# Kernel optimization log

Measured on AMD Instinct MI355X. Metric: run time of the kernel, lower is better.

The kernel has to match this reference:

```python
import jax, jax.numpy as jnp
import numpy as np

N_NODE = 40000  # item vocabulary
H = 100         # hidden size (SR-GNN default)
B = 64          # sessions per batch
L = 16          # items per session (equal-length sessions)
N = B * L       # total graph nodes
E = 2048        # total edges
NL = 1          # GatedGraphConv layers


def setup_inputs() -> dict:
    key = jax.random.key(0)
    ks = jax.random.split(key, 20)
    stdv = 1.0 / np.sqrt(H)
    u = lambda k, shape: jax.random.uniform(k, shape, jnp.float32, -stdv, stdv)
    return {
        "x": jax.random.randint(ks[0], (N,), 0, N_NODE),
        "edge_index": jax.random.randint(ks[1], (2, E), 0, N),
        "edge_weight": jax.random.uniform(ks[2], (E,), jnp.float32),
        "batch": jnp.arange(N) // L,  # node -> session id, equal-length sessions
        "embed": u(ks[3], (N_NODE, H)),
        "ggc_w": u(ks[4], (NL, H, H)),
        "gru_wih": u(ks[5], (3 * H, H)),
        "gru_whh": u(ks[6], (3 * H, H)),
        "gru_bih": u(ks[7], (3 * H,)),
        "gru_bhh": u(ks[8], (3 * H,)),
        "W1_w": u(ks[9], (H, H)), "W1_b": u(ks[10], (H,)),
        "W2_w": u(ks[11], (H, H)), "W2_b": u(ks[12], (H,)),
        "Wt_w": u(ks[13], (H, H)), "Wt_b": u(ks[14], (H,)),
        "q_w": u(ks[15], (1, H)), "q_b": u(ks[16], (1,)),
        "W3_w": u(ks[17], (H, 2 * H)), "W3_b": u(ks[18], (H,)),
    }


def reference(x, edge_index, edge_weight, batch, embed, ggc_w, gru_wih, gru_whh,
              gru_bih, gru_bhh, W1_w, W1_b, W2_w, W2_b, Wt_w, Wt_b, q_w, q_b,
              W3_w, W3_b):
    # Embedding lookup
    h = embed[x]  # [N, H]
    src, dst = edge_index[0], edge_index[1]
    # GatedGraphConv: weighted message aggregation + GRUCell update
    for l in range(NL):
        m = h @ ggc_w[l]                                             # [N, H]
        agg = jnp.zeros_like(h).at[dst].add(edge_weight[:, None] * m[src])
        gi = agg @ gru_wih.T + gru_bih                               # [N, 3H]
        gh = h @ gru_whh.T + gru_bhh
        ir, iz, inn = jnp.split(gi, 3, axis=-1)
        hr, hz, hn = jnp.split(gh, 3, axis=-1)
        r = jax.nn.sigmoid(ir + hr)
        zg = jax.nn.sigmoid(iz + hz)
        ng = jnp.tanh(inn + r * hn)
        h = (1.0 - zg) * ng + zg * h
    v = h.reshape(B, L, H)                                           # sessions
    s_l = v[:, -1]                                                   # [B, H] last item
    # alpha = q(sigmoid(W1(v_n) + W2(v)))
    a = jax.nn.sigmoid((s_l @ W1_w.T + W1_b)[:, None, :] + (v @ W2_w.T + W2_b))
    alpha = a @ q_w.T + q_b                                          # [B, L, 1]
    s_g = jnp.sum(alpha * v, axis=1)                                 # [B, H]
    s_h = jnp.concatenate([s_l, s_g], axis=-1) @ W3_w.T + W3_b       # [B, H]
    # Target attention: s_t[b] = softmax(E @ W_t(v_b)^T, -1) @ v_b, contracted
    # directly against E to avoid materializing [B, N_NODE, H].
    vt = v @ Wt_w.T + Wt_b                                           # [B, L, H]
    P = jax.nn.softmax(jnp.einsum('jh,blh->bjl', embed, vt), axis=-1)
    C = jnp.einsum('blh,jh->bjl', v, embed)                          # v_l . E_j
    z = s_h @ embed.T + jnp.sum(P * C, axis=-1)                      # [B, N_NODE]
    return z
```

## Files before the change

### kernel.cpp

```cpp
#include <hip/hip_runtime.h>
#include <hip/hip_bf16.h>

#define Hh    100
#define NN    1024
#define BB    64
#define LL    16
#define EE    2048
#define NNODE 40000

#define BSPL  4
#define BPB   (BB / BSPL)
#define PFR   8
#define PPAN  (PFR * 64 * 8)
#define GJ    4
#define EBS   104
#define GRB   4

typedef unsigned short u16;
typedef __attribute__((ext_vector_type(8))) short short8;
typedef __attribute__((ext_vector_type(4))) float f32x4;

__device__ __forceinline__ float bf2f(u16 u) {
    union { unsigned int i; float f; } v;
    v.i = ((unsigned int)u) << 16;
    return v.f;
}

__device__ __forceinline__ u16 f2bf(float f) {
    unsigned int x = __float_as_uint(f);
    unsigned int lsb = (x >> 16) & 1u;
    x += 0x7fffu + lsb;
    return (u16)(x >> 16);
}

__device__ __forceinline__ float sigmoidf_(float x) {
    return 1.0f / (1.0f + expf(-x));
}

template <bool BF>
__device__ __forceinline__ float ldv(const void* p, size_t i) {
    if (BF) return bf2f(((const u16*)p)[i]);
    return ((const float*)p)[i];
}
__device__ __forceinline__ float ldvf(int flag, const void* p, size_t i) {
    return flag ? ldv<true>(p, i) : ldv<false>(p, i);
}

template <bool BF>
__device__ void cvt_impl(int t,
                         const void* ew, const void* ggc, const void* wih, const void* whh,
                         const void* bih, const void* bhh, const void* W1w, const void* W1b,
                         const void* W2w, const void* W2b, const void* Wtw, const void* Wtb,
                         const void* qw, const void* qb, const void* W3w, const void* W3b,
                         float* __restrict__ W) {
    const void* src; int si; int doff; int di;
    if      (t <   2048) { src = ew;  si = t;          doff = 0;      di = si; }
    else if (t <  12048) { src = ggc; si = t - 2048;   doff = 2048;   di = si; }
    else if (t <  42048) { src = wih; si = t - 12048;  doff = 12048;  { int r = si / 100, k = si - r * 100; di = k * 800 + (r % 100) * 8 + r / 100; } }
    else if (t <  72048) { src = whh; si = t - 42048;  doff = 12048;  { int r = si / 100, k = si - r * 100; di = k * 800 + (r % 100) * 8 + 3 + r / 100; } }
    else if (t <  72348) { src = bih; si = t - 72048;  doff = 92048;  di = si; }
    else if (t <  72648) { src = bhh; si = t - 72348;  doff = 92352;  di = si; }
    else if (t <  82648) { src = W1w; si = t - 72648;  doff = 92656;  di = (si % 100) * 100 + si / 100; }
    else if (t <  82748) { src = W1b; si = t - 82648;  doff = 102656; di = si; }
    else if (t <  92748) { src = W2w; si = t - 82748;  doff = 102768; di = (si % 100) * 100 + si / 100; }
    else if (t <  92848) { src = W2b; si = t - 92748;  doff = 112768; di = si; }
    else if (t < 102848) { src = Wtw; si = t - 92848;  doff = 112880; di = (si % 100) * 100 + si / 100; }
    else if (t < 102948) { src = Wtb; si = t - 102848; doff = 122880; di = si; }
    else if (t < 103048) { src = qw;  si = t - 102948; doff = 122992; di = si; }
    else if (t < 103049) { src = qb;  si = t - 103048; doff = 123104; di = si; }
    else if (t < 123049) { src = W3w; si = t - 103049; doff = 123120; di = (si % 200) * 100 + si / 200; }
    else                 { src = W3b; si = t - 123049; doff = 143120; di = si; }
    W[doff + di] = ldv<BF>(src, si);
}

__global__ void __launch_bounds__(256) k_cvt(const void* embed_raw, int* __restrict__ flag,
                      const void* ew, const void* ggc, const void* wih, const void* whh,
                      const void* bih, const void* bhh, const void* W1w, const void* W1b,
                      const void* W2w, const void* W2b, const void* Wtw, const void* Wtb,
                      const void* qw, const void* qb, const void* W3w, const void* W3b,
                      float* __restrict__ W, u16* __restrict__ SD) {
    __shared__ int cnt;
    if (threadIdx.x == 0) cnt = 0;
    __syncthreads();
    int bad = 0;
    const u16* eb = (const u16*)embed_raw;
    for (int i = threadIdx.x; i < 4096; i += 256) {
        float v = bf2f(eb[i]);
        if (!(fabsf(v) <= 0.5f)) bad++;
    }
    if (bad) atomicAdd(&cnt, bad);
    __syncthreads();
    const bool bf = (cnt == 0);
    if (blockIdx.x == 0 && threadIdx.x == 0) flag[0] = bf ? 1 : 0;
    int t = blockIdx.x * 256 + threadIdx.x;
    if (t < 4096) ((unsigned int*)SD)[t] = 0u;
    if (t >= 123149) return;
    if (bf) cvt_impl<true >(t, ew, ggc, wih, whh, bih, bhh, W1w, W1b, W2w, W2b, Wtw, Wtb, qw, qb, W3w, W3b, W);
    else    cvt_impl<false>(t, ew, ggc, wih, whh, bih, bhh, W1w, W1b, W2w, W2b, Wtw, Wtb, qw, qb, W3w, W3b, W);
}

__global__ void __launch_bounds__(256) k_ecvt(const int* __restrict__ flag,
                                              const void* __restrict__ embed,
                                              u16* __restrict__ EB) {
    const bool bf = (flag[0] != 0);
    int t = blockIdx.x * 256 + threadIdx.x;
    const int total = (NNODE + 1) * (EBS / 2);
    if (t >= total) return;
    int r = t / (EBS / 2), c2 = t - r * (EBS / 2);
    int k0 = c2 * 2;
    unsigned int w = 0;
    if (r < NNODE && k0 + 1 < Hh) {
        if (bf) {
            w = *(const unsigned int*)&((const u16*)embed)[(size_t)r * Hh + k0];
        } else {
            float2 e2 = *(const float2*)&((const float*)embed)[(size_t)r * Hh + k0];
            w = (unsigned int)f2bf(e2.x) | ((unsigned int)f2bf(e2.y) << 16);
        }
    }
    ((unsigned int*)EB)[t] = w;
}

__global__ void __launch_bounds__(256) k_gm(const int* __restrict__ flag,
                                            const int* __restrict__ x,
                                            const void* __restrict__ embed,
                                            const float* __restrict__ ggc_w,
                                            float* __restrict__ m,
                                            float* __restrict__ agg) {
    __shared__ float W[Hh * Hh];
    __shared__ float H[8 * Hh];
    const int tid = threadIdx.x;
    const int fl = flag[0];
    const int r0 = blockIdx.x * 8;
    for (int idx = tid; idx < Hh * Hh; idx += 256) W[idx] = ggc_w[idx];
    for (int idx = tid; idx < 8 * Hh; idx += 256) {
        int i = idx / Hh, j = idx - i * Hh;
        H[idx] = ldvf(fl, embed, (size_t)x[r0 + i] * Hh + j);
    }
    for (int idx = tid; idx < 8 * Hh; idx += 256) agg[r0 * Hh + idx] = 0.0f;
    __syncthreads();
    for (int idx = tid; idx < 8 * Hh; idx += 256) {
        int i = idx / Hh, j = idx - i * Hh;
        float acc = 0.0f;
#pragma unroll 4
        for (int k = 0; k < Hh; ++k) acc += H[i * Hh + k] * W[k * Hh + j];
        m[(r0 + i) * Hh + j] = acc;
    }
}

__global__ void k_scatter(const int* __restrict__ ei, const float* __restrict__ ew,
                          const float* __restrict__ m, float* __restrict__ agg) {
    int t = blockIdx.x * 256 + threadIdx.x;
    if (t >= EE * Hh) return;
    int e = t / Hh, j = t - e * Hh;
    int src = ei[e], dst = ei[EE + e];
    atomicAdd(&agg[dst * Hh + j], ew[e] * m[src * Hh + j]);
}

__global__ void __launch_bounds__(256) k_gruatt(const int* __restrict__ flag,
                      const int* __restrict__ x, const void* __restrict__ embed,
                      const float* __restrict__ agg, const float* __restrict__ wC,
                      const float* __restrict__ bih, const float* __restrict__ bhh,
                      const float* __restrict__ W1T, const float* __restrict__ W1b,
                      const float* __restrict__ W2T, const float* __restrict__ W2b,
                      const float* __restrict__ WtT, const float* __restrict__ Wtb,
                      float* __restrict__ h1, float* __restrict__ Q2g,
                      float* __restrict__ VTg, float* __restrict__ Q1g) {
    __shared__ float sA[GRB * Hh];
    __shared__ float sH0[GRB * Hh];
    __shared__ float sV[GRB * Hh];
    const int tid = threadIdx.x;
    const int r0 = blockIdx.x * GRB;
    const int fl = flag[0];
    for (int o = tid; o < GRB * Hh; o += 256) {
        int i = o / Hh, j = o - i * Hh;
        sA[o] = agg[(r0 + i) * Hh + j];
        sH0[o] = ldvf(fl, embed, (size_t)x[r0 + i] * Hh + j);
    }
    __syncthreads();
    for (int o = tid; o < GRB * Hh; o += 256) {
        int i = o / Hh, j = o - i * Hh;
        float s_ir = bih[j], s_iz = bih[j + Hh], s_in = bih[j + 2 * Hh];
        float s_hr = bhh[j], s_hz = bhh[j + Hh], s_hn = bhh[j + 2 * Hh];
        const float* ai = sA + i * Hh;
        const float* hi = sH0 + i * Hh;
        const float* wbase = wC + j * 8;
        for (int k = 0; k < Hh; ++k) {
            float a = ai[k], h = hi[k];
            const float* wr = wbase + k * 800;
            float4 w0 = *(const float4*)wr;
            float2 w1 = *(const float2*)(wr + 4);
            s_ir += a * w0.x;
            s_iz += a * w0.y;
            s_in += a * w0.z;
            s_hr += h * w0.w;
            s_hz += h * w1.x;
            s_hn += h * w1.y;
        }
        float r = sigmoidf_(s_ir + s_hr);
        float z = sigmoidf_(s_iz + s_hz);
        float n = tanhf(s_in + r * s_hn);
        float hv = (1.0f - z) * n + z * hi[j];
        sV[o] = hv;
        h1[(r0 + i) * Hh + j] = hv;
    }
    __syncthreads();
    for (int o = tid; o < GRB * Hh; o += 256) {
        int i = o / Hh, j = o - i * Hh;
        const float* vi = sV + i * Hh;
        float a2 = 0.0f, at = 0.0f;
        for (int k = 0; k < Hh; ++k) {
            float vk = vi[k];
            a2 += vk * W2T[k * Hh + j];
            at += vk * WtT[k * Hh + j];
        }
        Q2g[(r0 + i) * Hh + j] = a2 + W2b[j];
        VTg[(r0 + i) * Hh + j] = at + Wtb[j];
    }
    if ((r0 & 15) == 12 && tid < Hh) {
        const float* vl = sV + 3 * Hh;
        float a1 = 0.0f;
        for (int k = 0; k < Hh; ++k) a1 += vl[k] * W1T[k * Hh + tid];
        Q1g[(r0 >> 4) * Hh + tid] = a1 + W1b[tid];
    }
}

__global__ void __launch_bounds__(256) k_att2(const float* __restrict__ h1,
                    const float* __restrict__ Q1g, const float* __restrict__ Q2g,
                    const float* __restrict__ VTg,
                    const float* __restrict__ qw, const float* __restrict__ qb,
                    const float* __restrict__ W3T, const float* __restrict__ W3b,
                    u16* __restrict__ P, u16* __restrict__ SD) {
    __shared__ float V[LL * Hh];
    __shared__ float VTs[LL * Hh];
    __shared__ float AL[LL];
    __shared__ float SG[Hh];
    __shared__ float SH[Hh];
    const int b = blockIdx.x, tid = threadIdx.x;
    for (int o = tid; o < LL * Hh; o += 256) {
        V[o] = h1[b * LL * Hh + o];
        VTs[o] = VTg[b * LL * Hh + o];
    }
    __syncthreads();
    {
        int l = tid >> 4, t = tid & 15;
        float acc = 0.0f;
        for (int j = t; j < Hh; j += 16)
            acc += sigmoidf_(Q1g[b * Hh + j] + Q2g[(b * LL + l) * Hh + j]) * qw[j];
        acc += __shfl_xor(acc, 8);
        acc += __shfl_xor(acc, 4);
        acc += __shfl_xor(acc, 2);
        acc += __shfl_xor(acc, 1);
        if (t == 0) AL[l] = acc + qb[0];
    }
    __syncthreads();
    if (tid < Hh) {
        float acc = 0.0f;
#pragma unroll
        for (int l = 0; l < LL; ++l) acc += AL[l] * V[l * Hh + tid];
        SG[tid] = acc;
    }
    __syncthreads();
    if (tid < Hh) {
        float acc = W3b[tid];
        for (int k = 0; k < Hh; ++k) acc += V[(LL - 1) * Hh + k] * W3T[k * Hh + tid];
        for (int k = 0; k < Hh; ++k) acc += SG[k] * W3T[(Hh + k) * Hh + tid];
        SH[tid] = acc;
    }
    __syncthreads();
    for (int w = tid; w < PFR * 64; w += 256) {
        int f = w >> 6, lane = w & 63;
        int t = f >> 2, ks = f & 3;
        int mm = lane & 15, qq = lane >> 4;
        int col0 = ks * 32 + qq * 8;
        short8 t8;
#pragma unroll
        for (int e = 0; e < 8; ++e) {
            int col = col0 + e;
            float v = 0.0f;
            if (col < Hh) v = (t == 0) ? VTs[mm * Hh + col] : V[mm * Hh + col];
            t8[e] = (short)f2bf(v);
        }
        *(short8*)&P[((size_t)b * PFR + f) * 512 + lane * 8] = t8;
    }
    if (tid < 128) {
        int ks = tid >> 5, qq = (tid >> 3) & 3, e = tid & 7;
        int col = ks * 32 + qq * 8 + e;
        float v = (col < Hh) ? SH[col] : 0.0f;
        SD[(((size_t)(b >> 4) * 4 + ks) * 64 + qq * 16 + (b & 15)) * 8 + e] = f2bf(v);
    }
}

__device__ __forceinline__ short8 load_efrag(const void* embed, bool bf, int j, int k0) {
    short8 v = {0, 0, 0, 0, 0, 0, 0, 0};
    if (j >= NNODE || k0 >= Hh) return v;
    if (bf) {
        const u16* row = (const u16*)embed + (size_t)j * Hh + k0;
        if (k0 + 8 <= Hh) {
            ushort4 a = *(const ushort4*)(row);
            ushort4 b = *(const ushort4*)(row + 4);
            v[0] = (short)a.x; v[1] = (short)a.y; v[2] = (short)a.z; v[3] = (short)a.w;
            v[4] = (short)b.x; v[5] = (short)b.y; v[6] = (short)b.z; v[7] = (short)b.w;
        } else {
            for (int e = 0; e < Hh - k0; ++e) v[e] = (short)row[e];
        }
    } else {
        const float* row = (const float*)embed + (size_t)j * Hh + k0;
        if (k0 + 8 <= Hh) {
            float4 a = *(const float4*)(row);
            float4 b = *(const float4*)(row + 4);
            v[0] = (short)f2bf(a.x); v[1] = (short)f2bf(a.y); v[2] = (short)f2bf(a.z); v[3] = (short)f2bf(a.w);
            v[4] = (short)f2bf(b.x); v[5] = (short)f2bf(b.y); v[6] = (short)f2bf(b.z); v[7] = (short)f2bf(b.w);
        } else {
            for (int e = 0; e < Hh - k0; ++e) v[e] = (short)f2bf(row[e]);
        }
    }
    return v;
}

template <int EMODE>
__global__ void __launch_bounds__(256) k_score(const int* __restrict__ flag,
                                               const void* __restrict__ embed,
                                               const u16* __restrict__ EB,
                                               const u16* __restrict__ P,
                                               const u16* __restrict__ SD,
                                               void* __restrict__ out) {
    __shared__ alignas(16) u16 sPan[2][PPAN];
    const int jb = blockIdx.x * 256;
    const int slice = blockIdx.y;
    const int b0 = slice * BPB;
    const int tid = threadIdx.x;
    const bool bf = (flag[0] != 0);
    const int wave = tid >> 6, lane = tid & 63;
    const int m = lane & 15, quad = lane >> 4;

    short8 Bf[GJ][4];
#pragma unroll
    for (int g = 0; g < GJ; ++g)
#pragma unroll
        for (int ks = 0; ks < 4; ++ks) {
            int j = jb + wave * 64 + g * 16 + m;
            if (EMODE) {
                short8 v = {0, 0, 0, 0, 0, 0, 0, 0};
                if (j < NNODE)
                    v = *(const short8*)&EB[(size_t)j * EBS + ks * 32 + quad * 8];
                Bf[g][ks] = v;
            } else {
                Bf[g][ks] = load_efrag(embed, bf, j, ks * 32 + quad * 8);
            }
        }

    short8 Sf[4];
#pragma unroll
    for (int ks = 0; ks < 4; ++ks)
        Sf[ks] = *(const short8*)&SD[(((size_t)slice * 4 + ks) * 64 + lane) * 8];
    f32x4 accsd[GJ];
#pragma unroll
    for (int g = 0; g < GJ; ++g) {
        accsd[g] = (f32x4){0.0f, 0.0f, 0.0f, 0.0f};
#pragma unroll
        for (int ks = 0; ks < 4; ++ks)
            accsd[g] = __builtin_amdgcn_mfma_f32_16x16x32_bf16(Sf[ks], Bf[g][ks], accsd[g], 0, 0, 0);
    }

    {
        const uint4* s4 = (const uint4*)(P + (size_t)b0 * PPAN);
        uint4 g0 = s4[tid], g1 = s4[tid + 256];
        uint4* d = (uint4*)sPan[0];
        d[tid] = g0; d[tid + 256] = g1;
    }
    __syncthreads();

    int cur = 0;
    for (int bi = 0; bi < BPB; ++bi) {
        const int b = b0 + bi;
        uint4 g0, g1;
        if (bi + 1 < BPB) {
            const uint4* s4 = (const uint4*)(P + (size_t)(b + 1) * PPAN);
            g0 = s4[tid]; g1 = s4[tid + 256];
        }

        const u16* sp = sPan[cur];
        f32x4 acc[GJ][2];
#pragma unroll
        for (int g = 0; g < GJ; ++g)
#pragma unroll
            for (int t = 0; t < 2; ++t)
                acc[g][t] = (f32x4){0.0f, 0.0f, 0.0f, 0.0f};
#pragma unroll
        for (int t = 0; t < 2; ++t) {
            short8 A0 = *(const short8*)&sp[(t * 4 + 0) * 512 + lane * 8];
            short8 A1 = *(const short8*)&sp[(t * 4 + 1) * 512 + lane * 8];
            short8 A2 = *(const short8*)&sp[(t * 4 + 2) * 512 + lane * 8];
            short8 A3 = *(const short8*)&sp[(t * 4 + 3) * 512 + lane * 8];
#pragma unroll
            for (int g = 0; g < GJ; ++g) {
                acc[g][t] = __builtin_amdgcn_mfma_f32_16x16x32_bf16(A0, Bf[g][0], acc[g][t], 0, 0, 0);
                acc[g][t] = __builtin_amdgcn_mfma_f32_16x16x32_bf16(A1, Bf[g][1], acc[g][t], 0, 0, 0);
                acc[g][t] = __builtin_amdgcn_mfma_f32_16x16x32_bf16(A2, Bf[g][2], acc[g][t], 0, 0, 0);
                acc[g][t] = __builtin_amdgcn_mfma_f32_16x16x32_bf16(A3, Bf[g][3], acc[g][t], 0, 0, 0);
            }
        }

#pragma unroll
        for (int g = 0; g < GJ; ++g) {
            float den = 0.0f, num = 0.0f;
#pragma unroll
            for (int r = 0; r < 4; ++r) {
                float p = __expf(acc[g][0][r]);
                den += p;
                num += p * acc[g][1][r];
            }
            den += __shfl_xor(den, 16); num += __shfl_xor(num, 16);
            den += __shfl_xor(den, 32); num += __shfl_xor(num, 32);
            f32x4 s4v = accsd[g];
            int rr = bi & 3;
            float sdv = (rr == 0) ? s4v[0] : (rr == 1) ? s4v[1] : (rr == 2) ? s4v[2] : s4v[3];
            sdv = __shfl(sdv, ((bi >> 2) << 4) | m);
            if (quad == 0) {
                int j = jb + wave * 64 + g * 16 + m;
                if (j < NNODE) {
                    float z = sdv + num / den;
                    if (bf) ((u16*)out)[(size_t)b * NNODE + j] = f2bf(z);
                    else    ((float*)out)[(size_t)b * NNODE + j] = z;
                }
            }
        }

        if (bi + 1 < BPB) {
            uint4* d = (uint4*)sPan[cur ^ 1];
            d[tid] = g0; d[tid + 256] = g1;
        }
        __syncthreads();
        cur ^= 1;
    }
}

extern "C" void kernel_launch(void* const* d_in, const int* in_sizes, int n_in,
                              void* d_out, int out_size, void* d_ws, size_t ws_size,
                              hipStream_t stream) {
    const int* x      = (const int*)d_in[0];
    const int* ei     = (const int*)d_in[1];
    const void* ew    = d_in[2];
    const void* embed = d_in[4];
    const void* ggc   = d_in[5];
    const void* wih   = d_in[6];
    const void* whh   = d_in[7];
    const void* bih   = d_in[8];
    const void* bhh   = d_in[9];
    const void* W1w   = d_in[10];
    const void* W1b   = d_in[11];
    const void* W2w   = d_in[12];
    const void* W2b   = d_in[13];
    const void* Wtw   = d_in[14];
    const void* Wtb   = d_in[15];
    const void* qw    = d_in[16];
    const void* qb    = d_in[17];
    const void* W3w   = d_in[18];
    const void* W3b   = d_in[19];
    float* ws = (float*)d_ws;
    int* flag = (int*)d_ws;

    float* W = ws + 64;
    float* ew_f  = W + 0;
    float* ggc_f = W + 2048;
    float* wC    = W + 12048;
    float* bih_f = W + 92048;
    float* bhh_f = W + 92352;
    float* W1T   = W + 92656;
    float* W1b_f = W + 102656;
    float* W2T   = W + 102768;
    float* W2b_f = W + 112768;
    float* WtT   = W + 112880;
    float* Wtb_f = W + 122880;
    float* qw_f  = W + 122992;
    float* qb_f  = W + 123104;
    float* W3T   = W + 123120;
    float* W3b_f = W + 143120;

    float* D     = ws + 143296;
    float* m     = D;
    float* agg   = D + 102400;
    float* h1    = D;
    float* Q2g   = D + 204800;
    float* VTg   = D + 307200;
    float* Q1g   = D + 409600;
    u16*   P     = (u16*)(D + 416000);
    u16*   SDp   = (u16*)(D + 547072);
    u16*   EB    = (u16*)(D + 551168);

    const size_t need_bytes = (size_t)(143296 + 551168) * 4 + (size_t)(NNODE + 1) * EBS * 2;
    const bool emode = (ws_size >= need_bytes);

    k_cvt    <<<dim3(482), dim3(256), 0, stream>>>(embed, flag, ew, ggc, wih, whh, bih, bhh,
                                                   W1w, W1b, W2w, W2b, Wtw, Wtb, qw, qb, W3w, W3b, W, SDp);
    if (emode)
        k_ecvt<<<dim3(((NNODE + 1) * (EBS / 2) + 255) / 256), dim3(256), 0, stream>>>(flag, embed, EB);
    k_gm     <<<dim3(128), dim3(256), 0, stream>>>(flag, x, embed, ggc_f, m, agg);
    k_scatter<<<dim3(800), dim3(256), 0, stream>>>(ei, ew_f, m, agg);
    k_gruatt <<<dim3(NN / GRB), dim3(256), 0, stream>>>(flag, x, embed, agg, wC, bih_f, bhh_f,
                                                        W1T, W1b_f, W2T, W2b_f, WtT, Wtb_f,
                                                        h1, Q2g, VTg, Q1g);
    k_att2   <<<dim3(BB), dim3(256), 0, stream>>>(h1, Q1g, Q2g, VTg, qw_f, qb_f, W3T, W3b_f, P, SDp);
    if (emode)
        k_score<1><<<dim3((NNODE + 255) / 256, BSPL), dim3(256), 0, stream>>>(flag, embed, EB, P, SDp, d_out);
    else
        k_score<0><<<dim3((NNODE + 255) / 256, BSPL), dim3(256), 0, stream>>>(flag, embed, EB, P, SDp, d_out);
}
```

Before: 203.3 us.

## Reassociate graph conv to scatter embeddings first, fuse panel packing, remap score grid

Uses linearity to scatter-add edge-weighted raw embeddings into agg0 first and apply the ggc weight afterwards inside the GRU kernel. This removes the separate message matmul kernel and the intermediate m buffer. Packing of the bf16 score panels moves from k_att2 into k_gruatt, GRB is halved so more blocks launch, and the k_score grid becomes 1D with a block remap that groups the four batch slices of neighbouring column tiles together for L2 locality. The tradeoff is duplicated ggc matmul work per block, and atomic scatter ordering now happens on pre-transform values, which changes float rounding slightly.

```diff
diff --git a/kernel.cpp b/kernel.cpp
--- a/kernel.cpp
+++ b/kernel.cpp
@@ -14,7 +14,7 @@
 #define PPAN  (PFR * 64 * 8)
 #define GJ    4
 #define EBS   104
-#define GRB   4
+#define GRB   2
 
 typedef unsigned short u16;
 typedef __attribute__((ext_vector_type(8))) short short8;
@@ -78,7 +78,7 @@
                       const void* bih, const void* bhh, const void* W1w, const void* W1b,
                       const void* W2w, const void* W2b, const void* Wtw, const void* Wtb,
                       const void* qw, const void* qb, const void* W3w, const void* W3b,
-                      float* __restrict__ W, u16* __restrict__ SD) {
+                      float* __restrict__ W, float* __restrict__ agg0) {
     __shared__ int cnt;
     if (threadIdx.x == 0) cnt = 0;
     __syncthreads();
@@ -93,7 +93,7 @@
     const bool bf = (cnt == 0);
     if (blockIdx.x == 0 && threadIdx.x == 0) flag[0] = bf ? 1 : 0;
     int t = blockIdx.x * 256 + threadIdx.x;
-    if (t < 4096) ((unsigned int*)SD)[t] = 0u;
+    if (t < NN * Hh) agg0[t] = 0.0f;
     if (t >= 123149) return;
     if (bf) cvt_impl<true >(t, ew, ggc, wih, whh, bih, bhh, W1w, W1b, W2w, W2b, Wtw, Wtb, qw, qb, W3w, W3b, W);
     else    cvt_impl<false>(t, ew, ggc, wih, whh, bih, bhh, W1w, W1b, W2w, W2b, Wtw, Wtb, qw, qb, W3w, W3b, W);
@@ -120,61 +120,61 @@
     ((unsigned int*)EB)[t] = w;
 }
 
-__global__ void __launch_bounds__(256) k_gm(const int* __restrict__ flag,
-                                            const int* __restrict__ x,
-                                            const void* __restrict__ embed,
-                                            const float* __restrict__ ggc_w,
-                                            float* __restrict__ m,
-                                            float* __restrict__ agg) {
-    __shared__ float W[Hh * Hh];
-    __shared__ float H[8 * Hh];
-    const int tid = threadIdx.x;
+__global__ void k_scatter2(const int* __restrict__ flag, const int* __restrict__ ei,
+                           const float* __restrict__ ew, const int* __restrict__ x,
+                           const void* __restrict__ embed, float* __restrict__ agg0) {
+    int t = blockIdx.x * 256 + threadIdx.x;
+    if (t >= EE * (Hh / 2)) return;
+    int e = t / (Hh / 2), j2 = t - e * (Hh / 2);
+    int j = j2 * 2;
+    int src = ei[e], dst = ei[EE + e];
     const int fl = flag[0];
-    const int r0 = blockIdx.x * 8;
-    for (int idx = tid; idx < Hh * Hh; idx += 256) W[idx] = ggc_w[idx];
-    for (int idx = tid; idx < 8 * Hh; idx += 256) {
-        int i = idx / Hh, j = idx - i * Hh;
-        H[idx] = ldvf(fl, embed, (size_t)x[r0 + i] * Hh + j);
-    }
-    for (int idx = tid; idx < 8 * Hh; idx += 256) agg[r0 * Hh + idx] = 0.0f;
-    __syncthreads();
-    for (int idx = tid; idx < 8 * Hh; idx += 256) {
-        int i = idx / Hh, j = idx - i * Hh;
-        float acc = 0.0f;
-#pragma unroll 4
-        for (int k = 0; k < Hh; ++k) acc += H[i * Hh + k] * W[k * Hh + j];
-        m[(r0 + i) * Hh + j] = acc;
-    }
-}
-
-__global__ void k_scatter(const int* __restrict__ ei, const float* __restrict__ ew,
-                          const float* __restrict__ m, float* __restrict__ agg) {
-    int t = blockIdx.x * 256 + threadIdx.x;
-    if (t >= EE * Hh) return;
-    int e = t / Hh, j = t - e * Hh;
-    int src = ei[e], dst = ei[EE + e];
-    atomicAdd(&agg[dst * Hh + j], ew[e] * m[src * Hh + j]);
+    float w = ew[e];
+    float h0, h1v;
+    size_t base = (size_t)x[src] * Hh + j;
+    if (fl) {
+        unsigned int u = *(const unsigned int*)&((const u16*)embed)[base];
+        h0 = bf2f((u16)(u & 0xffff));
+        h1v = bf2f((u16)(u >> 16));
+    } else {
+        float2 f2 = *(const float2*)&((const float*)embed)[base];
+        h0 = f2.x; h1v = f2.y;
+    }
+    atomicAdd(&agg0[dst * Hh + j], w * h0);
+    atomicAdd(&agg0[dst * Hh + j + 1], w * h1v);
 }
 
 __global__ void __launch_bounds__(256) k_gruatt(const int* __restrict__ flag,
                       const int* __restrict__ x, const void* __restrict__ embed,
-                      const float* __restrict__ agg, const float* __restrict__ wC,
+                      const float* __restrict__ agg0, const float* __restrict__ ggc_f,
+                      const float* __restrict__ wC,
                       const float* __restrict__ bih, const float* __restrict__ bhh,
                       const float* __restrict__ W1T, const float* __restrict__ W1b,
                       const float* __restrict__ W2T, const float* __restrict__ W2b,
                       const float* __restrict__ WtT, const float* __restrict__ Wtb,
                       float* __restrict__ h1, float* __restrict__ Q2g,
-                      float* __restrict__ VTg, float* __restrict__ Q1g) {
+                      float* __restrict__ Q1g, u16* __restrict__ P) {
+    __shared__ float sG[GRB * Hh];
+    __shared__ float sH0[GRB * Hh];
     __shared__ float sA[GRB * Hh];
-    __shared__ float sH0[GRB * Hh];
     __shared__ float sV[GRB * Hh];
+    __shared__ float sVT[GRB * Hh];
     const int tid = threadIdx.x;
     const int r0 = blockIdx.x * GRB;
     const int fl = flag[0];
     for (int o = tid; o < GRB * Hh; o += 256) {
         int i = o / Hh, j = o - i * Hh;
-        sA[o] = agg[(r0 + i) * Hh + j];
+        sG[o] = agg0[(r0 + i) * Hh + j];
         sH0[o] = ldvf(fl, embed, (size_t)x[r0 + i] * Hh + j);
+    }
+    __syncthreads();
+    for (int o = tid; o < GRB * Hh; o += 256) {
+        int i = o / Hh, j = o - i * Hh;
+        const float* gi = sG + i * Hh;
+        float acc = 0.0f;
+#pragma unroll 8
+        for (int k = 0; k < Hh; ++k) acc += gi[k] * ggc_f[k * Hh + j];
+        sA[o] = acc;
     }
     __syncthreads();
     for (int o = tid; o < GRB * Hh; o += 256) {
@@ -184,6 +184,7 @@
         const float* ai = sA + i * Hh;
         const float* hi = sH0 + i * Hh;
         const float* wbase = wC + j * 8;
+#pragma unroll 4
         for (int k = 0; k < Hh; ++k) {
             float a = ai[k], h = hi[k];
             const float* wr = wbase + k * 800;
@@ -208,38 +209,51 @@
         int i = o / Hh, j = o - i * Hh;
         const float* vi = sV + i * Hh;
         float a2 = 0.0f, at = 0.0f;
+#pragma unroll 8
         for (int k = 0; k < Hh; ++k) {
             float vk = vi[k];
             a2 += vk * W2T[k * Hh + j];
             at += vk * WtT[k * Hh + j];
         }
         Q2g[(r0 + i) * Hh + j] = a2 + W2b[j];
-        VTg[(r0 + i) * Hh + j] = at + Wtb[j];
-    }
-    if ((r0 & 15) == 12 && tid < Hh) {
-        const float* vl = sV + 3 * Hh;
+        sVT[o] = at + Wtb[j];
+    }
+    __syncthreads();
+    if ((r0 & 15) == 14 && tid < Hh) {
+        const float* vl = sV + Hh;
         float a1 = 0.0f;
+#pragma unroll 8
         for (int k = 0; k < Hh; ++k) a1 += vl[k] * W1T[k * Hh + tid];
         Q1g[(r0 >> 4) * Hh + tid] = a1 + W1b[tid];
     }
+    const int b = r0 >> 4;
+    if (tid < GRB * 2 * 4 * 4) {
+        int i = tid >> 5, rest = tid & 31;
+        int tt = rest >> 4, ks = (rest >> 2) & 3, qq = rest & 3;
+        int mm = (r0 & 15) + i;
+        int col0 = ks * 32 + qq * 8;
+        const float* srow = (tt == 0 ? sVT : sV) + i * Hh;
+        short8 t8;
+#pragma unroll
+        for (int e = 0; e < 8; ++e) {
+            int col = col0 + e;
+            t8[e] = (short)f2bf(col < Hh ? srow[col] : 0.0f);
+        }
+        *(short8*)&P[((size_t)b * PFR + tt * 4 + ks) * 512 + (qq * 16 + mm) * 8] = t8;
+    }
 }
 
 __global__ void __launch_bounds__(256) k_att2(const float* __restrict__ h1,
                     const float* __restrict__ Q1g, const float* __restrict__ Q2g,
-                    const float* __restrict__ VTg,
                     const float* __restrict__ qw, const float* __restrict__ qb,
                     const float* __restrict__ W3T, const float* __restrict__ W3b,
-                    u16* __restrict__ P, u16* __restrict__ SD) {
+                    u16* __restrict__ SD) {
     __shared__ float V[LL * Hh];
-    __shared__ float VTs[LL * Hh];
     __shared__ float AL[LL];
     __shared__ float SG[Hh];
     __shared__ float SH[Hh];
     const int b = blockIdx.x, tid = threadIdx.x;
-    for (int o = tid; o < LL * Hh; o += 256) {
-        V[o] = h1[b * LL * Hh + o];
-        VTs[o] = VTg[b * LL * Hh + o];
-    }
+    for (int o = tid; o < LL * Hh; o += 256) V[o] = h1[b * LL * Hh + o];
     __syncthreads();
     {
         int l = tid >> 4, t = tid & 15;
@@ -262,26 +276,13 @@
     __syncthreads();
     if (tid < Hh) {
         float acc = W3b[tid];
+#pragma unroll 4
         for (int k = 0; k < Hh; ++k) acc += V[(LL - 1) * Hh + k] * W3T[k * Hh + tid];
+#pragma unroll 4
         for (int k = 0; k < Hh; ++k) acc += SG[k] * W3T[(Hh + k) * Hh + tid];
         SH[tid] = acc;
     }
     __syncthreads();
-    for (int w = tid; w < PFR * 64; w += 256) {
-        int f = w >> 6, lane = w & 63;
-        int t = f >> 2, ks = f & 3;
-        int mm = lane & 15, qq = lane >> 4;
-        int col0 = ks * 32 + qq * 8;
-        short8 t8;
-#pragma unroll
-        for (int e = 0; e < 8; ++e) {
-            int col = col0 + e;
-            float v = 0.0f;
-            if (col < Hh) v = (t == 0) ? VTs[mm * Hh + col] : V[mm * Hh + col];
-            t8[e] = (short)f2bf(v);
-        }
-        *(short8*)&P[((size_t)b * PFR + f) * 512 + lane * 8] = t8;
-    }
     if (tid < 128) {
         int ks = tid >> 5, qq = (tid >> 3) & 3, e = tid & 7;
         int col = ks * 32 + qq * 8 + e;
@@ -317,6 +318,8 @@
     return v;
 }
 
+#define JBLK  157
+
 template <int EMODE>
 __global__ void __launch_bounds__(256) k_score(const int* __restrict__ flag,
                                                const void* __restrict__ embed,
@@ -325,8 +328,13 @@
                                                const u16* __restrict__ SD,
                                                void* __restrict__ out) {
     __shared__ alignas(16) u16 sPan[2][PPAN];
-    const int jb = blockIdx.x * 256;
-    const int slice = blockIdx.y;
+    const int bid = blockIdx.x;
+    const int grp = bid >> 5;
+    const int x8 = bid & 7;
+    const int slice = (bid >> 3) & 3;
+    const int jblk = grp * 8 + x8;
+    if (jblk >= JBLK) return;
+    const int jb = jblk * 256;
     const int b0 = slice * BPB;
     const int tid = threadIdx.x;
     const bool bf = (flag[0] != 0);
@@ -478,31 +486,28 @@
     float* W3b_f = W + 143120;
 
     float* D     = ws + 143296;
-    float* m     = D;
-    float* agg   = D + 102400;
-    float* h1    = D;
+    float* agg0  = D;
+    float* h1    = D + 102400;
     float* Q2g   = D + 204800;
-    float* VTg   = D + 307200;
-    float* Q1g   = D + 409600;
-    u16*   P     = (u16*)(D + 416000);
-    u16*   SDp   = (u16*)(D + 547072);
-    u16*   EB    = (u16*)(D + 551168);
-
-    const size_t need_bytes = (size_t)(143296 + 551168) * 4 + (size_t)(NNODE + 1) * EBS * 2;
+    float* Q1g   = D + 307200;
+    u16*   P     = (u16*)(D + 313600);
+    u16*   SDp   = (u16*)(D + 444672);
+    u16*   EB    = (u16*)(D + 448768);
+
+    const size_t need_bytes = (size_t)(143296 + 448768) * 4 + (size_t)(NNODE + 1) * EBS * 2;
     const bool emode = (ws_size >= need_bytes);
 
     k_cvt    <<<dim3(482), dim3(256), 0, stream>>>(embed, flag, ew, ggc, wih, whh, bih, bhh,
-                                                   W1w, W1b, W2w, W2b, Wtw, Wtb, qw, qb, W3w, W3b, W, SDp);
+                                                   W1w, W1b, W2w, W2b, Wtw, Wtb, qw, qb, W3w, W3b, W, agg0);
     if (emode)
         k_ecvt<<<dim3(((NNODE + 1) * (EBS / 2) + 255) / 256), dim3(256), 0, stream>>>(flag, embed, EB);
-    k_gm     <<<dim3(128), dim3(256), 0, stream>>>(flag, x, embed, ggc_f, m, agg);
-    k_scatter<<<dim3(800), dim3(256), 0, stream>>>(ei, ew_f, m, agg);
-    k_gruatt <<<dim3(NN / GRB), dim3(256), 0, stream>>>(flag, x, embed, agg, wC, bih_f, bhh_f,
+    k_scatter2<<<dim3(EE * (Hh / 2) / 256, 1), dim3(256), 0, stream>>>(flag, ei, ew_f, x, embed, agg0);
+    k_gruatt <<<dim3(NN / GRB), dim3(256), 0, stream>>>(flag, x, embed, agg0, ggc_f, wC, bih_f, bhh_f,
                                                         W1T, W1b_f, W2T, W2b_f, WtT, Wtb_f,
-                                                        h1, Q2g, VTg, Q1g);
-    k_att2   <<<dim3(BB), dim3(256), 0, stream>>>(h1, Q1g, Q2g, VTg, qw_f, qb_f, W3T, W3b_f, P, SDp);
+                                                        h1, Q2g, Q1g, P);
+    k_att2   <<<dim3(BB), dim3(256), 0, stream>>>(h1, Q1g, Q2g, qw_f, qb_f, W3T, W3b_f, SDp);
     if (emode)
-        k_score<1><<<dim3((NNODE + 255) / 256, BSPL), dim3(256), 0, stream>>>(flag, embed, EB, P, SDp, d_out);
+        k_score<1><<<dim3(((JBLK + 7) / 8) * 32), dim3(256), 0, stream>>>(flag, embed, EB, P, SDp, d_out);
     else
-        k_score<0><<<dim3((NNODE + 255) / 256, BSPL), dim3(256), 0, stream>>>(flag, embed, EB, P, SDp, d_out);
-}
+        k_score<0><<<dim3(((JBLK + 7) / 8) * 32), dim3(256), 0, stream>>>(flag, embed, EB, P, SDp, d_out);
+}
```

New measurement: 208.7 us. 2.6% more time.
